# Optimization experiments

Hardware: AMD Instinct MI355X
Metric: run time of the kernel (lower is better)

Reference implementation:

```python
import jax, jax.numpy as jnp
import numpy as np

DIM = 64
SHAPE = (1, DIM, 12, 12, 12)  # B, C, D, H, W


def setup_inputs() -> dict:
    key = jax.random.key(0)
    k1, k2, k3, k4 = jax.random.split(key, 4)
    x = jax.random.normal(k1, SHAPE, dtype=jnp.float32)
    # torch nn.Linear weights: [out, in]; scale like default init
    w_qkv = jax.random.normal(k2, (3 * DIM, DIM), dtype=jnp.float32) * (1.0 / np.sqrt(DIM))
    w_proj = jax.random.normal(k3, (DIM, DIM), dtype=jnp.float32) * (1.0 / np.sqrt(DIM))
    b_proj = jax.random.normal(k4, (DIM,), dtype=jnp.float32) * 0.01
    return {"x": x, "w_qkv": w_qkv, "w_proj": w_proj, "b_proj": b_proj}


def reference(x, w_qkv, w_proj, b_proj):
    B, C, D, H, W = x.shape
    num_heads = C // 2  # head_dim = 2, per module definition
    head_dim = C // num_heads
    scale = head_dim ** (-0.5)
    N = D * H * W

    # [B, N, C] token layout (permute channels last, flatten spatial)
    xt = jnp.transpose(x, (0, 2, 3, 4, 1)).reshape(B, N, C)
    qkv = xt @ w_qkv.T  # [B, N, 3C]
    qkv = qkv.reshape(B, N, 3, num_heads, head_dim).transpose(2, 0, 3, 1, 4)
    q, k, v = qkv[0], qkv[1], qkv[2]  # each [B, h, N, d]

    attn = jnp.einsum('bhqd,bhkd->bhqk', q, k) * scale  # materialized scores
    attn = jax.nn.softmax(attn, axis=-1)
    out = jnp.einsum('bhqk,bhkd->bhqd', attn, v)  # [B, h, N, d]
    out = out.transpose(0, 2, 1, 3).reshape(B, D, H, W, C)
    out = out @ w_proj.T + b_proj  # [B, D, H, W, C]
    return out
```

## Files before the change

kernel.cpp:

```cpp
#include <hip/hip_runtime.h>
#include <hip/hip_bf16.h>

#define N_TOK  1728
#define CDIM   64
#define NHEADS 32
#define NHT    54
#define NPAIR  (N_TOK / 2)
#define SEGS   8
#define SEGLEN (NPAIR / SEGS)
#define SEGSTR (SEGLEN + 1)
#define SCALE  0.70710678118654752f
#define LOG2E  1.44269504088896340736f
#define NBIAS  (-10.0f)

typedef _Float16 h2 __attribute__((ext_vector_type(2)));
typedef __fp16   hf2 __attribute__((ext_vector_type(2)));
union H2U { h2 h; hf2 hf; unsigned int u; };

__device__ __forceinline__ unsigned int pack2(float a, float b) {
    H2U c; c.h.x = (_Float16)a; c.h.y = (_Float16)b; return c.u;
}
__device__ __forceinline__ float hdot2a(unsigned int q, unsigned int k, float c) {
    H2U a, b; a.u = q; b.u = k;
#if __has_builtin(__builtin_amdgcn_fdot2)
    return __builtin_amdgcn_fdot2(a.h, b.h, c, false);
#else
    return fmaf((float)a.h.x, (float)b.h.x, fmaf((float)a.h.y, (float)b.h.y, c));
#endif
}
__device__ __forceinline__ float fd2(h2 a, h2 b, float c) {
#if __has_builtin(__builtin_amdgcn_fdot2)
    return __builtin_amdgcn_fdot2(a, b, c, false);
#else
    return fmaf((float)a.x, (float)b.x, fmaf((float)a.y, (float)b.y, c));
#endif
}
__device__ __forceinline__ unsigned int pk2u(float a, float b) {
#if __has_builtin(__builtin_amdgcn_cvt_pkrtz)
    H2U c; c.hf = __builtin_amdgcn_cvt_pkrtz(a, b); return c.u;
#else
    return pack2(a, b);
#endif
}

__device__ __forceinline__ float ldin(const void* p, int i, int f32) {
    if (f32) return ((const float*)p)[i];
    union { unsigned int b; float f; } c;
    c.b = ((unsigned int)((const unsigned short*)p)[i]) << 16;
    return c.f;
}
__device__ __forceinline__ int sniff_f32(const void* x) {
    union { unsigned int b; float f; } c;
    c.b = ((unsigned int)((const unsigned short*)x)[threadIdx.x & 63]) << 16;
    int bad = (((c.b >> 23) & 0xFF) == 0xFF) || (fabsf(c.f) > 1e10f);
    return (__ballot(bad) != 0ULL) ? 1 : 0;
}

__global__ void __launch_bounds__(64)
qkv_pack(const void* __restrict__ xv, const void* __restrict__ wv,
         unsigned int* __restrict__ Qp, unsigned int* __restrict__ KVg) {
    const int f     = sniff_f32(xv);
    const int lane  = threadIdx.x;
    const int h     = blockIdx.y & 31;
    const int which = blockIdx.y >> 5;
    const int r0    = (which << 6) + 2 * h;
    const int n     = blockIdx.x * 64 + lane;
    float a0 = 0.f, a1 = 0.f;
    if (f) {
        const float* x  = (const float*)xv;
        const float* w0 = (const float*)wv + r0 * CDIM;
        const float* w1 = w0 + CDIM;
#pragma unroll 8
        for (int c = 0; c < CDIM; ++c) {
            float xc = x[c * N_TOK + n];
            a0 = fmaf(xc, w0[c], a0);
            a1 = fmaf(xc, w1[c], a1);
        }
    } else {
#pragma unroll 8
        for (int c = 0; c < CDIM; ++c) {
            float xc = ldin(xv, c * N_TOK + n, 0);
            a0 = fmaf(xc, ldin(wv, r0 * CDIM + c, 0), a0);
            a1 = fmaf(xc, ldin(wv, (r0 + 1) * CDIM + c, 0), a1);
        }
    }
    if (which == 0) {
        Qp[h * N_TOK + n] = pack2(a0 * (SCALE * LOG2E), a1 * (SCALE * LOG2E));
    } else if (which == 1) {
        KVg[(h * NPAIR + (n >> 1)) * 4 + (n & 1)] = pack2(a0, a1);
    } else {
        float b0 = __shfl_xor(a0, 1);
        float b1 = __shfl_xor(a1, 1);
        unsigned int val = (n & 1) ? pack2(b1, a1)
                                   : pack2(a0, b0);
        KVg[(h * NPAIR + (n >> 1)) * 4 + 2 + (n & 1)] = val;
    }
}

__global__ void __launch_bounds__(256, 8)
attn_kernel(const unsigned int* __restrict__ Qp, const uint4* __restrict__ KVg,
            float* __restrict__ O) {
    __shared__ uint4 KVs[SEGS * SEGSTR];
    __shared__ float redbuf[4 * 32 * 3];
    const int tid  = threadIdx.x;
    const int lane = tid & 63;
    const int wav  = tid >> 6;
    const int ht   = blockIdx.x;
    const int h    = blockIdx.y;
    const int t0   = ht * 32;
    const int q    = lane & 31;
    const int seg  = (wav << 1) | (lane >> 5);

    for (int e = tid; e < NPAIR; e += 256)
        KVs[(e / SEGLEN) * SEGSTR + (e % SEGLEN)] = KVg[h * NPAIR + e];
    const unsigned int qh = Qp[h * N_TOK + t0 + q];
    __syncthreads();

    const uint4* KVp = &KVs[seg * SEGSTR];
    const float nb = NBIAS;
    H2U one2; one2.u = 0x3C003C00u;
    float l0 = 0.f, l1 = 0.f, l2 = 0.f, l3 = 0.f;
    float p0 = 0.f, p1 = 0.f, p2 = 0.f, p3 = 0.f;
    float s0 = 0.f, s1 = 0.f, s2 = 0.f, s3 = 0.f;
#pragma unroll
    for (int g = 0; g < SEGLEN; g += 4) {
        uint4 d0 = KVp[g], d1 = KVp[g + 1], d2 = KVp[g + 2], d3 = KVp[g + 3];
        float ea, eb; H2U pe, vz, vw;

        ea = __builtin_amdgcn_exp2f(hdot2a(qh, d0.x, nb));
        eb = __builtin_amdgcn_exp2f(hdot2a(qh, d0.y, nb));
        pe.u = pk2u(ea, eb);
        vz.u = d0.z; vw.u = d0.w;
        l0 = fd2(pe.h, one2.h, l0);
        p0 = fd2(pe.h, vz.h, p0);
        s0 = fd2(pe.h, vw.h, s0);

        ea = __builtin_amdgcn_exp2f(hdot2a(qh, d1.x, nb));
        eb = __builtin_amdgcn_exp2f(hdot2a(qh, d1.y, nb));
        pe.u = pk2u(ea, eb);
        vz.u = d1.z; vw.u = d1.w;
        l1 = fd2(pe.h, one2.h, l1);
        p1 = fd2(pe.h, vz.h, p1);
        s1 = fd2(pe.h, vw.h, s1);

        ea = __builtin_amdgcn_exp2f(hdot2a(qh, d2.x, nb));
        eb = __builtin_amdgcn_exp2f(hdot2a(qh, d2.y, nb));
        pe.u = pk2u(ea, eb);
        vz.u = d2.z; vw.u = d2.w;
        l2 = fd2(pe.h, one2.h, l2);
        p2 = fd2(pe.h, vz.h, p2);
        s2 = fd2(pe.h, vw.h, s2);

        ea = __builtin_amdgcn_exp2f(hdot2a(qh, d3.x, nb));
        eb = __builtin_amdgcn_exp2f(hdot2a(qh, d3.y, nb));
        pe.u = pk2u(ea, eb);
        vz.u = d3.z; vw.u = d3.w;
        l3 = fd2(pe.h, one2.h, l3);
        p3 = fd2(pe.h, vz.h, p3);
        s3 = fd2(pe.h, vw.h, s3);
    }
    float L = (l0 + l1) + (l2 + l3);
    float A = (p0 + p1) + (p2 + p3);
    float B = (s0 + s1) + (s2 + s3);
    L += __shfl_xor(L, 32); A += __shfl_xor(A, 32); B += __shfl_xor(B, 32);
    if (lane < 32) {
        float* r = redbuf + wav * 96 + q * 3;
        r[0] = L; r[1] = A; r[2] = B;
    }
    __syncthreads();
    if (wav == 0 && lane < 32) {
        float Lt = 0.f, At = 0.f, Bt = 0.f;
#pragma unroll
        for (int w = 0; w < 4; ++w) {
            const float* r = redbuf + w * 96 + q * 3;
            Lt += r[0]; At += r[1]; Bt += r[2];
        }
        float inv = 1.0f / Lt;
        *((float2*)(O + (t0 + q) * CDIM + 2 * h)) =
            make_float2(At * inv, Bt * inv);
    }
}

__global__ void __launch_bounds__(256)
proj_kernel(const void* __restrict__ xv,
            const float* __restrict__ O,
            const void* __restrict__ w_proj, const void* __restrict__ b_proj,
            void* __restrict__ out) {
    __shared__ float Ws[CDIM * 65];
    const int f    = sniff_f32(xv);
    const int tid  = threadIdx.x;
    const int lane = tid & 63;
    const int wav  = tid >> 6;
    for (int e = tid; e < CDIM * CDIM; e += 256)
        Ws[(e & 63) * 65 + (e >> 6)] = ldin(w_proj, e, f);
    __syncthreads();
    int n = blockIdx.x * 4 + wav;
    float acc = ldin(b_proj, lane, f);
#pragma unroll 8
    for (int ci = 0; ci < CDIM; ++ci)
        acc = fmaf(O[n * CDIM + ci],
                   Ws[ci * 65 + lane], acc);
    if (f) ((float*)out)[n * CDIM + lane] = acc;
    else   ((__hip_bfloat16*)out)[n * CDIM + lane] = __float2bfloat16(acc);
}

extern "C" void kernel_launch(void* const* d_in, const int* in_sizes, int n_in,
                              void* d_out, int out_size, void* d_ws, size_t ws_size,
                              hipStream_t stream) {
    const void* x      = d_in[0];
    const void* w_qkv  = d_in[1];
    const void* w_proj = d_in[2];
    const void* b_proj = d_in[3];

    float*        O   = (float*)d_ws;
    unsigned int* Qp  = (unsigned int*)(O + N_TOK * CDIM);
    unsigned int* KVg = Qp + NHEADS * N_TOK;

    qkv_pack   <<<dim3(27, 96), 64, 0, stream>>>(x, w_qkv, Qp, KVg);
    attn_kernel<<<dim3(NHT, NHEADS), 256, 0, stream>>>(Qp, (const uint4*)KVg, O);
    proj_kernel<<<432, 256, 0, stream>>>(x, O, w_proj, b_proj, d_out);
}
```

Measured before the change: 90.66 us.

## Read K/V directly from global memory with 64 queries per block, no LDS staging

The attention kernel stops staging each head's K/V pairs into shared memory and instead has each wave read its quarter of the keys straight from global memory. Loads are wave-uniform, so they can go through the scalar/constant cache. Each block now covers 64 queries (one per lane) across 4 key segments instead of 32 queries across 8 half-wave segments, which halves the grid and the redundant K/V staging per head. The inner loop is no longer fully unrolled and the bias is pinned in a VGPR. The risks are global/scalar load latency in the inner loop and fewer blocks in flight.

```diff
diff --git a/kernel.cpp b/kernel.cpp
--- a/kernel.cpp
+++ b/kernel.cpp
@@ -4,11 +4,10 @@
 #define N_TOK  1728
 #define CDIM   64
 #define NHEADS 32
-#define NHT    54
+#define NQT    27
 #define NPAIR  (N_TOK / 2)
-#define SEGS   8
+#define SEGS   4
 #define SEGLEN (NPAIR / SEGS)
-#define SEGSTR (SEGLEN + 1)
 #define SCALE  0.70710678118654752f
 #define LOG2E  1.44269504088896340736f
 #define NBIAS  (-10.0f)
@@ -97,34 +96,28 @@
     }
 }
 
-__global__ void __launch_bounds__(256, 8)
+__global__ void __launch_bounds__(256, 4)
 attn_kernel(const unsigned int* __restrict__ Qp, const uint4* __restrict__ KVg,
             float* __restrict__ O) {
-    __shared__ uint4 KVs[SEGS * SEGSTR];
-    __shared__ float redbuf[4 * 32 * 3];
+    __shared__ float redbuf[SEGS * 193];
     const int tid  = threadIdx.x;
     const int lane = tid & 63;
-    const int wav  = tid >> 6;
-    const int ht   = blockIdx.x;
+    const int wav  = __builtin_amdgcn_readfirstlane(tid >> 6);
+    const int qt   = blockIdx.x;
     const int h    = blockIdx.y;
-    const int t0   = ht * 32;
-    const int q    = lane & 31;
-    const int seg  = (wav << 1) | (lane >> 5);
-
-    for (int e = tid; e < NPAIR; e += 256)
-        KVs[(e / SEGLEN) * SEGSTR + (e % SEGLEN)] = KVg[h * NPAIR + e];
-    const unsigned int qh = Qp[h * N_TOK + t0 + q];
-    __syncthreads();
-
-    const uint4* KVp = &KVs[seg * SEGSTR];
-    const float nb = NBIAS;
+    const int t0   = qt * 64;
+
+    const unsigned int qh = Qp[h * N_TOK + t0 + lane];
+    const uint4* __restrict__ Kp = KVg + h * NPAIR + wav * SEGLEN;
+
+    float nb = NBIAS;
+    asm("" : "+v"(nb));
     H2U one2; one2.u = 0x3C003C00u;
     float l0 = 0.f, l1 = 0.f, l2 = 0.f, l3 = 0.f;
     float p0 = 0.f, p1 = 0.f, p2 = 0.f, p3 = 0.f;
     float s0 = 0.f, s1 = 0.f, s2 = 0.f, s3 = 0.f;
-#pragma unroll
     for (int g = 0; g < SEGLEN; g += 4) {
-        uint4 d0 = KVp[g], d1 = KVp[g + 1], d2 = KVp[g + 2], d3 = KVp[g + 3];
+        uint4 d0 = Kp[g], d1 = Kp[g + 1], d2 = Kp[g + 2], d3 = Kp[g + 3];
         float ea, eb; H2U pe, vz, vw;
 
         ea = __builtin_amdgcn_exp2f(hdot2a(qh, d0.x, nb));
@@ -162,21 +155,20 @@
     float L = (l0 + l1) + (l2 + l3);
     float A = (p0 + p1) + (p2 + p3);
     float B = (s0 + s1) + (s2 + s3);
-    L += __shfl_xor(L, 32); A += __shfl_xor(A, 32); B += __shfl_xor(B, 32);
-    if (lane < 32) {
-        float* r = redbuf + wav * 96 + q * 3;
+    {
+        float* r = redbuf + wav * 193 + lane * 3;
         r[0] = L; r[1] = A; r[2] = B;
     }
     __syncthreads();
-    if (wav == 0 && lane < 32) {
+    if (wav == 0) {
         float Lt = 0.f, At = 0.f, Bt = 0.f;
 #pragma unroll
-        for (int w = 0; w < 4; ++w) {
-            const float* r = redbuf + w * 96 + q * 3;
+        for (int w = 0; w < SEGS; ++w) {
+            const float* r = redbuf + w * 193 + lane * 3;
             Lt += r[0]; At += r[1]; Bt += r[2];
         }
         float inv = 1.0f / Lt;
-        *((float2*)(O + (t0 + q) * CDIM + 2 * h)) =
+        *((float2*)(O + (t0 + lane) * CDIM + 2 * h)) =
             make_float2(At * inv, Bt * inv);
     }
 }
@@ -217,6 +209,6 @@
     unsigned int* KVg = Qp + NHEADS * N_TOK;
 
     qkv_pack   <<<dim3(27, 96), 64, 0, stream>>>(x, w_qkv, Qp, KVg);
-    attn_kernel<<<dim3(NHT, NHEADS), 256, 0, stream>>>(Qp, (const uint4*)KVg, O);
+    attn_kernel<<<dim3(NQT, NHEADS), 256, 0, stream>>>(Qp, (const uint4*)KVg, O);
     proj_kernel<<<432, 256, 0, stream>>>(x, O, w_proj, b_proj, d_out);
 }
```

New measurement: 98.19 us. 1.08x slower.
